# Kernel tuning notes

Hardware: AMD Instinct MI355X
Metric: run time of the kernel (lower is better)

Reference implementation:

```python
import jax, jax.numpy as jnp
import numpy as np

D_MODEL = 2048
N_Q = 16
N_KV = 4
HEAD_DIM = 128
WINDOW = 512
ROPE_BASE = 10000.0


def _rope_cos_sin(T, dtype):
    half = HEAD_DIM // 2
    inv_freq = 1.0 / (ROPE_BASE ** (jnp.arange(0, half, dtype=jnp.float32) * 2.0 / HEAD_DIM))
    pos = jnp.arange(T, dtype=jnp.float32)
    ang = pos[:, None] * inv_freq[None, :]            # [T, half]
    emb = jnp.concatenate([ang, ang], axis=-1)        # [T, HEAD_DIM]
    return jnp.cos(emb).astype(dtype), jnp.sin(emb).astype(dtype)


def _rotate_half(x):
    x1, x2 = jnp.split(x, 2, axis=-1)
    return jnp.concatenate([-x2, x1], axis=-1)


def _apply_rope(t, cos, sin):
    # t: [B, H, T, hd]; cos/sin: [T, hd]
    return t * cos[None, None, :, :] + _rotate_half(t) * sin[None, None, :, :]


def setup_inputs() -> dict:
    key = jax.random.key(0)
    ks = jax.random.split(key, 5)
    s = 0.02
    return {
        "x": jax.random.normal(ks[0], (2, 2048, D_MODEL), dtype=jnp.float32),
        "wq": jax.random.normal(ks[1], (D_MODEL, N_Q * HEAD_DIM), dtype=jnp.float32) * s,
        "wk": jax.random.normal(ks[2], (D_MODEL, N_KV * HEAD_DIM), dtype=jnp.float32) * s,
        "wv": jax.random.normal(ks[3], (D_MODEL, N_KV * HEAD_DIM), dtype=jnp.float32) * s,
        "wo": jax.random.normal(ks[4], (N_Q * HEAD_DIM, D_MODEL), dtype=jnp.float32) * s,
    }


def reference(x, wq, wk, wv, wo):
    B, T, _ = x.shape
    q = (x @ wq).reshape(B, T, N_Q, HEAD_DIM).transpose(0, 2, 1, 3)    # [B,Hq,T,hd]
    k = (x @ wk).reshape(B, T, N_KV, HEAD_DIM).transpose(0, 2, 1, 3)   # [B,Hkv,T,hd]
    v = (x @ wv).reshape(B, T, N_KV, HEAD_DIM).transpose(0, 2, 1, 3)

    cos, sin = _rope_cos_sin(T, x.dtype)
    q = _apply_rope(q, cos, sin)
    k = _apply_rope(k, cos, sin)

    # GQA: repeat_interleave kv heads to match q heads
    g = N_Q // N_KV
    k = jnp.repeat(k, g, axis=1)
    v = jnp.repeat(v, g, axis=1)

    scale = 1.0 / np.sqrt(HEAD_DIM)
    scores = jnp.einsum("bhqd,bhkd->bhqk", q, k) * scale

    idx = jnp.arange(T)
    diff = idx[:, None] - idx[None, :]
    keep = (diff >= 0) & (diff < WINDOW)               # causal & sliding window
    scores = jnp.where(keep[None, None, :, :], scores, jnp.finfo(scores.dtype).min)
    attn = jax.nn.softmax(scores, axis=-1)

    out = jnp.einsum("bhqk,bhkd->bhqd", attn, v)       # [B,Hq,T,hd]
    out = out.transpose(0, 2, 1, 3).reshape(B, T, N_Q * HEAD_DIM)
    return out @ wo
```

## Files before the change

### kernel.cpp

```cpp
#include <hip/hip_runtime.h>

#define T_SEQ   2048
#define DM      2048
#define N_Q     16
#define N_KV    4
#define HD      128
#define WIN     512
#define NB      2
#define NQKV    3072
#define QK_SCALE_L2E 0.12751744f

typedef short bf16x8 __attribute__((ext_vector_type(8)));
typedef float f32x4  __attribute__((ext_vector_type(4)));
typedef unsigned short us4v __attribute__((ext_vector_type(4)));

__device__ __forceinline__ unsigned short f2bf(float f) {
    union { float f; unsigned u; } v; v.f = f;
    unsigned u = v.u;
    u += 0x7fffu + ((u >> 16) & 1u);
    return (unsigned short)(u >> 16);
}
__device__ __forceinline__ float bf2f(unsigned short h) {
    union { unsigned u; float f; } v; v.u = ((unsigned)h) << 16;
    return v.f;
}
__device__ __forceinline__ unsigned cvt_pk_bf16(float a, float b) {
    unsigned r;
    asm("v_cvt_pk_bf16_f32 %0, %1, %2" : "=v"(r) : "v"(a), "v"(b));
    return r;
}

#define GLOAD_LDS16(g, l) __builtin_amdgcn_global_load_lds( \
    (const __attribute__((address_space(1))) void*)(g),     \
    (__attribute__((address_space(3))) void*)(l), 16, 0, 0)


struct us4 { unsigned short a, b, c, d; };

__global__ __launch_bounds__(256)
void f32_to_bf16_vec(const float* __restrict__ in, unsigned short* __restrict__ out, long n) {
    long i = ((long)blockIdx.x * 256 + threadIdx.x) * 4;
    if (i < n) {
        float4 f = *(const float4*)(in + i);
        us4 o; o.a = f2bf(f.x); o.b = f2bf(f.y); o.c = f2bf(f.z); o.d = f2bf(f.w);
        *(us4*)(out + i) = o;
    }
}

__global__ __launch_bounds__(256)
void transpose_w_all(const float* __restrict__ wq, const float* __restrict__ wk,
                     const float* __restrict__ wv, const float* __restrict__ wo,
                     unsigned short* __restrict__ wqkvT, unsigned short* __restrict__ woT) {
    __shared__ float tile[32][33];
    const int z = blockIdx.z;
    const float* in; unsigned short* out; int C;
    if (z == 0)      { in = wq; out = wqkvT;                        C = DM;  }
    else if (z == 1) { in = wk; out = wqkvT + (long)DM * DM;        C = 512; }
    else if (z == 2) { in = wv; out = wqkvT + (long)(DM + 512) * DM; C = 512; }
    else             { in = wo; out = woT;                          C = DM;  }
    const int c0 = blockIdx.x * 32, r0 = blockIdx.y * 32;
    if (c0 >= C) return;
    const int tx = threadIdx.x, ty = threadIdx.y;
#pragma unroll
    for (int i = 0; i < 4; ++i)
        tile[ty + i * 8][tx] = in[(long)(r0 + ty + i * 8) * C + c0 + tx];
    __syncthreads();
#pragma unroll
    for (int i = 0; i < 4; ++i)
        out[(long)(c0 + ty + i * 8) * DM + r0 + tx] = f2bf(tile[tx][ty + i * 8]);
}

__global__ __launch_bounds__(256)
void rope_table(float* __restrict__ cosT, float* __restrict__ sinT) {
    const int idx = blockIdx.x * 256 + threadIdx.x;
    const int t = idx >> 6, d = idx & 63;
    const float inv = __expf(-(float)d * (9.210340371976184f / 64.0f));
    const float ang = (float)t * inv;
    cosT[idx] = cosf(ang);
    sinT[idx] = sinf(ang);
}

__global__ __launch_bounds__(256)
void rope_apply(unsigned short* __restrict__ qkv,
                const float* __restrict__ cosT, const float* __restrict__ sinT) {
    const int idx = blockIdx.x * 256 + threadIdx.x;
    const int d4 = (idx & 15) * 4;
    const int hh = (idx >> 4) % 20;
    const int row = idx / (16 * 20);
    const int t = row & (T_SEQ - 1);
    const int col = (hh < N_Q) ? hh * HD + d4 : DM + (hh - N_Q) * HD + d4;
    unsigned short* p = qkv + (long)row * NQKV + col;
    us4v a = *(const us4v*)p;
    us4v b = *(const us4v*)(p + 64);
    float4 c = *(const float4*)&cosT[t * 64 + d4];
    float4 s = *(const float4*)&sinT[t * 64 + d4];
    const float sc = (hh < N_Q) ? QK_SCALE_L2E : 1.0f;
    us4v o1, o2;
    const float cc[4] = { c.x, c.y, c.z, c.w }, ss[4] = { s.x, s.y, s.z, s.w };
#pragma unroll
    for (int i = 0; i < 4; ++i) {
        const float av = bf2f(a[i]), bv = bf2f(b[i]);
        o1[i] = f2bf((av * cc[i] - bv * ss[i]) * sc);
        o2[i] = f2bf((bv * cc[i] + av * ss[i]) * sc);
    }
    *(us4v*)p        = o1;
    *(us4v*)(p + 64) = o2;
}

__global__ __launch_bounds__(256)
void transpose_v(const unsigned short* __restrict__ qkv, unsigned short* __restrict__ vt) {
    __shared__ unsigned short tile[32][33];
    const int bh = blockIdx.z;
    const int d0 = blockIdx.y * 32;
    const int t0 = blockIdx.x * 32;
    const int tx = threadIdx.x, ty = threadIdx.y;
    const long inbase = (long)(bh >> 2) * T_SEQ;
    const int coff = DM + N_KV * HD + (bh & 3) * HD;
#pragma unroll
    for (int i = 0; i < 4; ++i)
        tile[ty + i * 8][tx] = qkv[(inbase + t0 + ty + i * 8) * NQKV + coff + d0 + tx];
    __syncthreads();
#pragma unroll
    for (int i = 0; i < 4; ++i)
        vt[((long)bh * HD + d0 + ty + i * 8) * T_SEQ + t0 + tx] = tile[tx][ty + i * 8];
}


template<int OUT_BF16>
__global__ __launch_bounds__(256)
void gemm_bt(const unsigned short* __restrict__ A,
             const unsigned short* __restrict__ Bt,
             void* __restrict__ Cvoid, int K, int ldc) {
    __shared__ __align__(16) unsigned short sA[128 * 64];
    __shared__ __align__(16) unsigned short sB[128 * 64];
    const int tid = threadIdx.x;
    const int lane = tid & 63;
    const int wid = tid >> 6;
    const int wr = (wid >> 1) * 64, wc = (wid & 1) * 64;

    const int gx = gridDim.x;
    const int nwg = gx * gridDim.y;
    int flat = blockIdx.y * gx + blockIdx.x;
    flat = (flat & 7) * (nwg >> 3) + (flat >> 3);
    const long Arow0 = (long)(flat / gx) * 128;
    const long Brow0 = (long)(flat % gx) * 128;

    f32x4 acc[4][4] = {};

    for (int kt = 0; kt < K; kt += 64) {
        __syncthreads();
#pragma unroll
        for (int n = 0; n < 4; ++n) {
            const int linb = n * 256 + wid * 64;
            const int lin  = linb + lane;
            const int row  = lin >> 3;
            const int sc   = (lin & 7) ^ (row & 7);
            const unsigned short* gA = A  + (Arow0 + row) * K + kt + sc * 8;
            const unsigned short* gB = Bt + (Brow0 + row) * K + kt + sc * 8;
            GLOAD_LDS16(gA, &sA[linb * 8]);
            GLOAD_LDS16(gB, &sB[linb * 8]);
        }
        __syncthreads();
#pragma unroll
        for (int kk = 0; kk < 2; ++kk) {
            bf16x8 av[4], bv[4];
#pragma unroll
            for (int i = 0; i < 4; ++i) {
                const int row = wr + i * 16 + (lane & 15);
                const int c = (kk * 4 + (lane >> 4)) ^ (row & 7);
                av[i] = *(const bf16x8*)&sA[row * 64 + c * 8];
            }
#pragma unroll
            for (int j = 0; j < 4; ++j) {
                const int row = wc + j * 16 + (lane & 15);
                const int c = (kk * 4 + (lane >> 4)) ^ (row & 7);
                bv[j] = *(const bf16x8*)&sB[row * 64 + c * 8];
            }
#pragma unroll
            for (int i = 0; i < 4; ++i)
#pragma unroll
                for (int j = 0; j < 4; ++j)
                    acc[i][j] = __builtin_amdgcn_mfma_f32_16x16x32_bf16(av[i], bv[j], acc[i][j], 0, 0, 0);
        }
    }

    const int r0 = (int)Arow0 + wr + ((lane >> 4) << 2);
    const int c0 = (int)Brow0 + wc + (lane & 15);
    if (OUT_BF16) {
        unsigned short* C = (unsigned short*)Cvoid;
#pragma unroll
        for (int i = 0; i < 4; ++i)
#pragma unroll
            for (int j = 0; j < 4; ++j)
#pragma unroll
                for (int r = 0; r < 4; ++r)
                    C[(long)(r0 + i * 16 + r) * ldc + c0 + j * 16] = f2bf(acc[i][j][r]);
    } else {
        float* C = (float*)Cvoid;
#pragma unroll
        for (int i = 0; i < 4; ++i)
#pragma unroll
            for (int j = 0; j < 4; ++j)
#pragma unroll
                for (int r = 0; r < 4; ++r)
                    C[(long)(r0 + i * 16 + r) * ldc + c0 + j * 16] = acc[i][j][r];
    }
}


__global__ __launch_bounds__(512, 2)
void attn_kernel(const unsigned short* __restrict__ qkv,
                 const unsigned short* __restrict__ vt,
                 unsigned short* __restrict__ aout) {
    const int qt = blockIdx.x, hkv = blockIdx.y, b = blockIdx.z;
    const int tid = threadIdx.x, lane = tid & 63, w = tid >> 6;
    const int qh = hkv * 4 + (w & 3);
    const int qsub = w >> 2;
    const int q0w = qt * 64 + qsub * 32;
    const int lo = lane & 15, hi = lane >> 4;

    __shared__ __align__(16) unsigned short sK[2][64 * 128];
    __shared__ __align__(16) unsigned short sV[2][128 * 64];
    __shared__ __align__(16) unsigned short plds[8][32 * 64];
    unsigned short* pl = plds[w];

    bf16x8 qf2[2][4];
#pragma unroll
    for (int f = 0; f < 2; ++f) {
        const unsigned short* qp = qkv + (long)(b * T_SEQ + q0w + f * 16 + lo) * NQKV + qh * HD + hi * 8;
#pragma unroll
        for (int s = 0; s < 4; ++s) qf2[f][s] = *(const bf16x8*)(qp + s * 32);
    }

    f32x4 of[8][2] = {};
    float m_r[2] = { -1e30f, -1e30f };
    float s_r[2] = { 0.f, 0.f };

    int kstart = qt * 64 - (WIN - 1);
    if (kstart < 0) kstart = 0;
    kstart &= ~63;
    const int kend = qt * 64 + 63;

    const unsigned short* kbase = qkv + (long)b * T_SEQ * NQKV + DM + hkv * HD;
    const unsigned short* vbase = vt + (long)(b * N_KV + hkv) * HD * T_SEQ;

    int kr[2], kc[2], vr[2], vc[2];
#pragma unroll
    for (int u = 0; u < 2; ++u) {
        const int c = u * 512 + tid;
        kr[u] = c >> 4;  kc[u] = (c & 15) ^ (kr[u] & 7);
        vr[u] = c >> 3;  vc[u] = (c & 7) ^ (vr[u] & 7);
    }

#define STAGE(bf, kt_) do {                                                              \
    _Pragma("unroll")                                                                    \
    for (int u = 0; u < 2; ++u) {                                                        \
        const int dbase = (u * 512 + w * 64) * 8;                                        \
        GLOAD_LDS16(kbase + (long)((kt_) + kr[u]) * NQKV + kc[u] * 8, &sK[bf][dbase]);   \
        GLOAD_LDS16(vbase + (long)vr[u] * T_SEQ + (kt_) + vc[u] * 8, &sV[bf][dbase]);    \
    } } while (0)

    STAGE(0, kstart);
    asm volatile("s_waitcnt vmcnt(0)" ::: "memory");
    __syncthreads();

    int buf = 0;
    for (int kt = kstart; kt <= kend; kt += 64) {
        if (kt + 64 <= kend) STAGE(buf ^ 1, kt + 64);

        f32x4 sf[4][2] = {};
        __builtin_amdgcn_s_setprio(1);
#pragma unroll
        for (int n = 0; n < 4; ++n) {
            const int row = n * 16 + lo;
#pragma unroll
            for (int s = 0; s < 4; ++s) {
                const int c = (s * 4 + hi) ^ (row & 7);
                bf16x8 kf = *(const bf16x8*)&sK[buf][row * 128 + c * 8];
                sf[n][0] = __builtin_amdgcn_mfma_f32_16x16x32_bf16(kf, qf2[0][s], sf[n][0], 0, 0, 0);
                sf[n][1] = __builtin_amdgcn_mfma_f32_16x16x32_bf16(kf, qf2[1][s], sf[n][1], 0, 0, 0);
            }
        }
        __builtin_amdgcn_s_setprio(0);

        float pv[2][4][4];
        float mx[2] = { -1e30f, -1e30f };
#pragma unroll
        for (int f = 0; f < 2; ++f) {
            const int q = q0w + f * 16 + lo;
#pragma unroll
            for (int n = 0; n < 4; ++n)
#pragma unroll
                for (int r = 0; r < 4; ++r) {
                    const int d = q - (kt + n * 16 + hi * 4 + r);
                    pv[f][n][r] = (d >= 0 && d < WIN) ? sf[n][f][r] : -1e30f;
                    mx[f] = fmaxf(mx[f], pv[f][n][r]);
                }
            mx[f] = fmaxf(mx[f], __shfl_xor(mx[f], 16));
            mx[f] = fmaxf(mx[f], __shfl_xor(mx[f], 32));
        }

        const bool ok = (mx[0] <= m_r[0] + 8.0f) && (mx[1] <= m_r[1] + 8.0f);
        if (!__all(ok)) {
#pragma unroll
            for (int f = 0; f < 2; ++f) {
                const float mnew = fmaxf(m_r[f], mx[f]);
                const float resc = exp2f(m_r[f] - mnew);
                s_r[f] *= resc;
                m_r[f] = mnew;
                float r4[4];
#pragma unroll
                for (int r = 0; r < 4; ++r) r4[r] = __shfl(resc, hi * 4 + r);
#pragma unroll
                for (int j = 0; j < 8; ++j) {
                    of[j][f][0] *= r4[0]; of[j][f][1] *= r4[1];
                    of[j][f][2] *= r4[2]; of[j][f][3] *= r4[3];
                }
            }
        }

#pragma unroll
        for (int f = 0; f < 2; ++f) {
            float psum = 0.f;
#pragma unroll
            for (int n = 0; n < 4; ++n)
#pragma unroll
                for (int r = 0; r < 4; ++r) {
                    pv[f][n][r] = exp2f(pv[f][n][r] - m_r[f]);
                    psum += pv[f][n][r];
                }
            psum += __shfl_xor(psum, 16);
            psum += __shfl_xor(psum, 32);
            s_r[f] += psum;
        }

        const int swz = (lo & 7) << 3;
#pragma unroll
        for (int f = 0; f < 2; ++f) {
            const int rowq = f * 16 + lo;
#pragma unroll
            for (int n = 0; n < 4; ++n) {
                const int k0 = n * 16 + hi * 4;
                *(unsigned*)&pl[rowq * 64 + (k0 ^ swz)]       = cvt_pk_bf16(pv[f][n][0], pv[f][n][1]);
                *(unsigned*)&pl[rowq * 64 + ((k0 + 2) ^ swz)] = cvt_pk_bf16(pv[f][n][2], pv[f][n][3]);
            }
        }
        asm volatile("s_waitcnt lgkmcnt(0)" ::: "memory");
        __builtin_amdgcn_sched_barrier(0);
        bf16x8 pa2[2][2];
#pragma unroll
        for (int f = 0; f < 2; ++f)
#pragma unroll
            for (int ks = 0; ks < 2; ++ks) {
                const int c = (ks * 4 + hi) ^ (lo & 7);
                pa2[f][ks] = *(const bf16x8*)&pl[(f * 16 + lo) * 64 + c * 8];
            }

        __builtin_amdgcn_s_setprio(1);
#pragma unroll
        for (int j = 0; j < 8; ++j) {
            const int row = j * 16 + lo;
#pragma unroll
            for (int ks = 0; ks < 2; ++ks) {
                const int c = (ks * 4 + hi) ^ (row & 7);
                bf16x8 vf = *(const bf16x8*)&sV[buf][row * 64 + c * 8];
                of[j][0] = __builtin_amdgcn_mfma_f32_16x16x32_bf16(pa2[0][ks], vf, of[j][0], 0, 0, 0);
                of[j][1] = __builtin_amdgcn_mfma_f32_16x16x32_bf16(pa2[1][ks], vf, of[j][1], 0, 0, 0);
            }
        }
        __builtin_amdgcn_s_setprio(0);

        asm volatile("s_waitcnt vmcnt(0)" ::: "memory");
        __syncthreads();
        buf ^= 1;
    }
#undef STAGE

#pragma unroll
    for (int f = 0; f < 2; ++f) {
        float s4[4];
#pragma unroll
        for (int r = 0; r < 4; ++r) s4[r] = __shfl(s_r[f], hi * 4 + r);
#pragma unroll
        for (int r = 0; r < 4; ++r) {
            const int qrow = q0w + f * 16 + hi * 4 + r;
            const float inv = 1.0f / s4[r];
            unsigned short* op = aout + (long)(b * T_SEQ + qrow) * DM + qh * HD + lo;
#pragma unroll
            for (int j = 0; j < 8; ++j) op[j * 16] = f2bf(of[j][f][r] * inv);
        }
    }
}


extern "C" void kernel_launch(void* const* d_in, const int* in_sizes, int n_in,
                              void* d_out, int out_size, void* d_ws, size_t ws_size,
                              hipStream_t stream) {
    (void)in_sizes; (void)n_in; (void)out_size; (void)ws_size;
    const float* x  = (const float*)d_in[0];
    const float* wq = (const float*)d_in[1];
    const float* wk = (const float*)d_in[2];
    const float* wv = (const float*)d_in[3];
    const float* wo = (const float*)d_in[4];
    float* out = (float*)d_out;
    char* ws = (char*)d_ws;

    unsigned short* xbf   = (unsigned short*)(ws);
    unsigned short* wqkvT = (unsigned short*)(ws + 16777216);
    unsigned short* woT   = (unsigned short*)(ws + 29360128);
    unsigned short* qkv   = (unsigned short*)(ws + 37748736);
    unsigned short* vt    = (unsigned short*)(ws + 62914560);
    unsigned short* aout  = (unsigned short*)(ws + 67108864);
    float* cosT = (float*)(ws + 83886080);
    float* sinT = (float*)(ws + 84410368);

    const long Mx = (long)NB * T_SEQ * DM;
    f32_to_bf16_vec<<<dim3(8192), dim3(256), 0, stream>>>(x, xbf, Mx);
    transpose_w_all<<<dim3(64, 64, 4), dim3(32, 8), 0, stream>>>(wq, wk, wv, wo, wqkvT, woT);
    rope_table<<<dim3(512), dim3(256), 0, stream>>>(cosT, sinT);

    gemm_bt<1><<<dim3(NQKV / 128, 32), dim3(256), 0, stream>>>(xbf, wqkvT, qkv, DM, NQKV);
    rope_apply<<<dim3(5120), dim3(256), 0, stream>>>(qkv, cosT, sinT);
    transpose_v<<<dim3(64, 4, 8), dim3(32, 8), 0, stream>>>(qkv, vt);
    attn_kernel<<<dim3(32, 4, 2), dim3(512), 0, stream>>>(qkv, vt, aout);
    gemm_bt<0><<<dim3(DM / 128, 32), dim3(256), 0, stream>>>(aout, woT, out, DM, DM);
}
```

Before: 174.6 us.

## Merge prep kernels into two launches and split attention into 32-row tiles

The three input-prep kernels (x cast, weight transposes, rope table) become one flat-grid kernel, and rope_apply plus the V transpose become a second one, which cuts launch count. The attention kernel moves from 512-thread blocks covering 64 query rows to 256-thread blocks covering 32 rows, which doubles the grid to 512 blocks for better CU fill. The cost is that each K/V tile is now loaded by twice as many blocks, and with 32-row tiles the sliding window spans more 64-key tiles per query row, so total K/V traffic grows.

```diff
diff --git a/kernel.cpp b/kernel.cpp
--- a/kernel.cpp
+++ b/kernel.cpp
@@ -34,45 +34,45 @@
     (const __attribute__((address_space(1))) void*)(g),     \
     (__attribute__((address_space(3))) void*)(l), 16, 0, 0)
 
-
 struct us4 { unsigned short a, b, c, d; };
 
+
 __global__ __launch_bounds__(256)
-void f32_to_bf16_vec(const float* __restrict__ in, unsigned short* __restrict__ out, long n) {
-    long i = ((long)blockIdx.x * 256 + threadIdx.x) * 4;
-    if (i < n) {
-        float4 f = *(const float4*)(in + i);
+void prep_a(const float* __restrict__ x, const float* __restrict__ wq,
+            const float* __restrict__ wk, const float* __restrict__ wv,
+            const float* __restrict__ wo,
+            unsigned short* __restrict__ xbf, unsigned short* __restrict__ wqkvT,
+            unsigned short* __restrict__ woT,
+            float* __restrict__ cosT, float* __restrict__ sinT) {
+    __shared__ float tile[32][33];
+    int blk = blockIdx.x;
+    if (blk < 8192) {
+        long i = ((long)blk * 256 + threadIdx.x) * 4;
+        float4 f = *(const float4*)(x + i);
         us4 o; o.a = f2bf(f.x); o.b = f2bf(f.y); o.c = f2bf(f.z); o.d = f2bf(f.w);
-        *(us4*)(out + i) = o;
-    }
-}
-
-__global__ __launch_bounds__(256)
-void transpose_w_all(const float* __restrict__ wq, const float* __restrict__ wk,
-                     const float* __restrict__ wv, const float* __restrict__ wo,
-                     unsigned short* __restrict__ wqkvT, unsigned short* __restrict__ woT) {
-    __shared__ float tile[32][33];
-    const int z = blockIdx.z;
-    const float* in; unsigned short* out; int C;
-    if (z == 0)      { in = wq; out = wqkvT;                        C = DM;  }
-    else if (z == 1) { in = wk; out = wqkvT + (long)DM * DM;        C = 512; }
-    else if (z == 2) { in = wv; out = wqkvT + (long)(DM + 512) * DM; C = 512; }
-    else             { in = wo; out = woT;                          C = DM;  }
-    const int c0 = blockIdx.x * 32, r0 = blockIdx.y * 32;
-    if (c0 >= C) return;
-    const int tx = threadIdx.x, ty = threadIdx.y;
-#pragma unroll
-    for (int i = 0; i < 4; ++i)
-        tile[ty + i * 8][tx] = in[(long)(r0 + ty + i * 8) * C + c0 + tx];
-    __syncthreads();
-#pragma unroll
-    for (int i = 0; i < 4; ++i)
-        out[(long)(c0 + ty + i * 8) * DM + r0 + tx] = f2bf(tile[tx][ty + i * 8]);
-}
-
-__global__ __launch_bounds__(256)
-void rope_table(float* __restrict__ cosT, float* __restrict__ sinT) {
-    const int idx = blockIdx.x * 256 + threadIdx.x;
+        *(us4*)(xbf + i) = o;
+        return;
+    }
+    blk -= 8192;
+    if (blk < 10240) {
+        const float* in; unsigned short* outp; int C, bx, by;
+        if (blk < 4096)      { in = wq; outp = wqkvT;                         C = DM;  bx = blk & 63;          by = blk >> 6; }
+        else if (blk < 5120) { int k = blk - 4096; in = wk; outp = wqkvT + (long)DM * DM;         C = 512; bx = k & 15; by = k >> 4; }
+        else if (blk < 6144) { int k = blk - 5120; in = wv; outp = wqkvT + (long)(DM + 512) * DM; C = 512; bx = k & 15; by = k >> 4; }
+        else                 { int k = blk - 6144; in = wo; outp = woT;                           C = DM;  bx = k & 63; by = k >> 6; }
+        const int c0 = bx * 32, r0 = by * 32;
+        const int tx = threadIdx.x & 31, ty = threadIdx.x >> 5;
+#pragma unroll
+        for (int i = 0; i < 4; ++i)
+            tile[ty + i * 8][tx] = in[(long)(r0 + ty + i * 8) * C + c0 + tx];
+        __syncthreads();
+#pragma unroll
+        for (int i = 0; i < 4; ++i)
+            outp[(long)(c0 + ty + i * 8) * DM + r0 + tx] = f2bf(tile[tx][ty + i * 8]);
+        return;
+    }
+    blk -= 10240;
+    const int idx = blk * 256 + threadIdx.x;
     const int t = idx >> 6, d = idx & 63;
     const float inv = __expf(-(float)d * (9.210340371976184f / 64.0f));
     const float ang = (float)t * inv;
@@ -80,49 +80,52 @@
     sinT[idx] = sinf(ang);
 }
 
+
 __global__ __launch_bounds__(256)
-void rope_apply(unsigned short* __restrict__ qkv,
-                const float* __restrict__ cosT, const float* __restrict__ sinT) {
-    const int idx = blockIdx.x * 256 + threadIdx.x;
-    const int d4 = (idx & 15) * 4;
-    const int hh = (idx >> 4) % 20;
-    const int row = idx / (16 * 20);
-    const int t = row & (T_SEQ - 1);
-    const int col = (hh < N_Q) ? hh * HD + d4 : DM + (hh - N_Q) * HD + d4;
-    unsigned short* p = qkv + (long)row * NQKV + col;
-    us4v a = *(const us4v*)p;
-    us4v b = *(const us4v*)(p + 64);
-    float4 c = *(const float4*)&cosT[t * 64 + d4];
-    float4 s = *(const float4*)&sinT[t * 64 + d4];
-    const float sc = (hh < N_Q) ? QK_SCALE_L2E : 1.0f;
-    us4v o1, o2;
-    const float cc[4] = { c.x, c.y, c.z, c.w }, ss[4] = { s.x, s.y, s.z, s.w };
-#pragma unroll
-    for (int i = 0; i < 4; ++i) {
-        const float av = bf2f(a[i]), bv = bf2f(b[i]);
-        o1[i] = f2bf((av * cc[i] - bv * ss[i]) * sc);
-        o2[i] = f2bf((bv * cc[i] + av * ss[i]) * sc);
-    }
-    *(us4v*)p        = o1;
-    *(us4v*)(p + 64) = o2;
-}
-
-__global__ __launch_bounds__(256)
-void transpose_v(const unsigned short* __restrict__ qkv, unsigned short* __restrict__ vt) {
-    __shared__ unsigned short tile[32][33];
-    const int bh = blockIdx.z;
-    const int d0 = blockIdx.y * 32;
-    const int t0 = blockIdx.x * 32;
-    const int tx = threadIdx.x, ty = threadIdx.y;
+void prep_b(unsigned short* __restrict__ qkv,
+            const float* __restrict__ cosT, const float* __restrict__ sinT,
+            unsigned short* __restrict__ vt) {
+    __shared__ unsigned short stile[32][33];
+    int blk = blockIdx.x;
+    if (blk < 5120) {
+        const int idx = blk * 256 + threadIdx.x;
+        const int d4 = (idx & 15) * 4;
+        const int hh = (idx >> 4) % 20;
+        const int row = idx / (16 * 20);
+        const int t = row & (T_SEQ - 1);
+        const int col = (hh < N_Q) ? hh * HD + d4 : DM + (hh - N_Q) * HD + d4;
+        unsigned short* p = qkv + (long)row * NQKV + col;
+        us4v a = *(const us4v*)p;
+        us4v b = *(const us4v*)(p + 64);
+        float4 c = *(const float4*)&cosT[t * 64 + d4];
+        float4 s = *(const float4*)&sinT[t * 64 + d4];
+        const float sc = (hh < N_Q) ? QK_SCALE_L2E : 1.0f;
+        us4v o1, o2;
+        const float cc[4] = { c.x, c.y, c.z, c.w }, ss[4] = { s.x, s.y, s.z, s.w };
+#pragma unroll
+        for (int i = 0; i < 4; ++i) {
+            const float av = bf2f(a[i]), bv = bf2f(b[i]);
+            o1[i] = f2bf((av * cc[i] - bv * ss[i]) * sc);
+            o2[i] = f2bf((bv * cc[i] + av * ss[i]) * sc);
+        }
+        *(us4v*)p        = o1;
+        *(us4v*)(p + 64) = o2;
+        return;
+    }
+    blk -= 5120;
+    const int bh = blk >> 8;
+    const int d0 = ((blk >> 6) & 3) * 32;
+    const int t0 = (blk & 63) * 32;
+    const int tx = threadIdx.x & 31, ty = threadIdx.x >> 5;
     const long inbase = (long)(bh >> 2) * T_SEQ;
     const int coff = DM + N_KV * HD + (bh & 3) * HD;
 #pragma unroll
     for (int i = 0; i < 4; ++i)
-        tile[ty + i * 8][tx] = qkv[(inbase + t0 + ty + i * 8) * NQKV + coff + d0 + tx];
+        stile[ty + i * 8][tx] = qkv[(inbase + t0 + ty + i * 8) * NQKV + coff + d0 + tx];
     __syncthreads();
 #pragma unroll
     for (int i = 0; i < 4; ++i)
-        vt[((long)bh * HD + d0 + ty + i * 8) * T_SEQ + t0 + tx] = tile[tx][ty + i * 8];
+        vt[((long)bh * HD + d0 + ty + i * 8) * T_SEQ + t0 + tx] = stile[tx][ty + i * 8];
 }
 
 
@@ -208,20 +211,19 @@
 }
 
 
-__global__ __launch_bounds__(512, 2)
+__global__ __launch_bounds__(256)
 void attn_kernel(const unsigned short* __restrict__ qkv,
                  const unsigned short* __restrict__ vt,
                  unsigned short* __restrict__ aout) {
     const int qt = blockIdx.x, hkv = blockIdx.y, b = blockIdx.z;
     const int tid = threadIdx.x, lane = tid & 63, w = tid >> 6;
-    const int qh = hkv * 4 + (w & 3);
-    const int qsub = w >> 2;
-    const int q0w = qt * 64 + qsub * 32;
+    const int qh = hkv * 4 + w;
+    const int q0w = qt * 32;
     const int lo = lane & 15, hi = lane >> 4;
 
     __shared__ __align__(16) unsigned short sK[2][64 * 128];
     __shared__ __align__(16) unsigned short sV[2][128 * 64];
-    __shared__ __align__(16) unsigned short plds[8][32 * 64];
+    __shared__ __align__(16) unsigned short plds[4][32 * 64];
     unsigned short* pl = plds[w];
 
     bf16x8 qf2[2][4];
@@ -236,26 +238,26 @@
     float m_r[2] = { -1e30f, -1e30f };
     float s_r[2] = { 0.f, 0.f };
 
-    int kstart = qt * 64 - (WIN - 1);
+    int kstart = q0w - (WIN - 1);
     if (kstart < 0) kstart = 0;
     kstart &= ~63;
-    const int kend = qt * 64 + 63;
+    const int kend = q0w + 31;
 
     const unsigned short* kbase = qkv + (long)b * T_SEQ * NQKV + DM + hkv * HD;
     const unsigned short* vbase = vt + (long)(b * N_KV + hkv) * HD * T_SEQ;
 
-    int kr[2], kc[2], vr[2], vc[2];
-#pragma unroll
-    for (int u = 0; u < 2; ++u) {
-        const int c = u * 512 + tid;
+    int kr[4], kc[4], vr[4], vc[4];
+#pragma unroll
+    for (int u = 0; u < 4; ++u) {
+        const int c = u * 256 + tid;
         kr[u] = c >> 4;  kc[u] = (c & 15) ^ (kr[u] & 7);
         vr[u] = c >> 3;  vc[u] = (c & 7) ^ (vr[u] & 7);
     }
 
 #define STAGE(bf, kt_) do {                                                              \
     _Pragma("unroll")                                                                    \
-    for (int u = 0; u < 2; ++u) {                                                        \
-        const int dbase = (u * 512 + w * 64) * 8;                                        \
+    for (int u = 0; u < 4; ++u) {                                                        \
+        const int dbase = (u * 256 + w * 64) * 8;                                        \
         GLOAD_LDS16(kbase + (long)((kt_) + kr[u]) * NQKV + kc[u] * 8, &sK[bf][dbase]);   \
         GLOAD_LDS16(vbase + (long)vr[u] * T_SEQ + (kt_) + vc[u] * 8, &sV[bf][dbase]);    \
     } } while (0)
@@ -414,14 +416,9 @@
     float* cosT = (float*)(ws + 83886080);
     float* sinT = (float*)(ws + 84410368);
 
-    const long Mx = (long)NB * T_SEQ * DM;
-    f32_to_bf16_vec<<<dim3(8192), dim3(256), 0, stream>>>(x, xbf, Mx);
-    transpose_w_all<<<dim3(64, 64, 4), dim3(32, 8), 0, stream>>>(wq, wk, wv, wo, wqkvT, woT);
-    rope_table<<<dim3(512), dim3(256), 0, stream>>>(cosT, sinT);
-
+    prep_a<<<dim3(18944), dim3(256), 0, stream>>>(x, wq, wk, wv, wo, xbf, wqkvT, woT, cosT, sinT);
     gemm_bt<1><<<dim3(NQKV / 128, 32), dim3(256), 0, stream>>>(xbf, wqkvT, qkv, DM, NQKV);
-    rope_apply<<<dim3(5120), dim3(256), 0, stream>>>(qkv, cosT, sinT);
-    transpose_v<<<dim3(64, 4, 8), dim3(32, 8), 0, stream>>>(qkv, vt);
-    attn_kernel<<<dim3(32, 4, 2), dim3(512), 0, stream>>>(qkv, vt, aout);
+    prep_b<<<dim3(7168), dim3(256), 0, stream>>>(qkv, cosT, sinT, vt);
+    attn_kernel<<<dim3(T_SEQ / 32, 4, 2), dim3(256), 0, stream>>>(qkv, vt, aout);
     gemm_bt<0><<<dim3(DM / 128, 32), dim3(256), 0, stream>>>(aout, woT, out, DM, DM);
 }
```

Measured after the change: 187.7 us (median of 4 runs). 1.08x slower.
